# Kernel optimization log

Hardware: AMD Instinct MI355X
Metric: run time of the kernel (lower is better)

## Reference

```python
import jax, jax.numpy as jnp
import numpy as np
from jax import lax

BS, K, N = 8, 8, 16            # batch, gathers per sample, picks per curve
T, WG = 3072, 64               # gather time samples, traces
H, WC = 256, 256               # CVEncoder ScaleSize
RH, RW = 1024, 512             # resize (also GatherEncoder outLen=RH)
T0, T1 = 0.0, 7000.0           # tInt[0], tInt[-1]


def setup_inputs() -> dict:
    key = jax.random.key(0)
    ks = jax.random.split(key, 8)
    gather = jax.random.normal(ks[0], (BS, K, T, WG), jnp.float32)
    # cv: times sorted, strictly > 0, within [T0, T1]; velocities within VMM range
    times = jnp.sort(jax.random.uniform(ks[1], (BS, K, N), minval=100.0, maxval=T1), axis=-1)
    vels = jnp.sort(jax.random.uniform(ks[2], (BS, K, N), minval=1500.0, maxval=4500.0), axis=-1)
    cv = jnp.stack([times, vels], axis=-1).astype(jnp.float32)
    VMM = jnp.tile(jnp.array([1500.0, 4500.0], jnp.float32), (BS, 1))
    def cw(k, shape):
        return (jax.random.normal(k, shape, jnp.float32) * 0.1)
    params = dict(
        w1=cw(ks[3], (1, 1, 3, 3)), b1=jnp.zeros((1,), jnp.float32), g1=jnp.ones((1,), jnp.float32), be1=jnp.zeros((1,), jnp.float32),
        w2=cw(ks[4], (2, 3, 3, 3)), b2=jnp.zeros((2,), jnp.float32), g2=jnp.ones((2,), jnp.float32), be2=jnp.zeros((2,), jnp.float32),
        w3=cw(ks[5], (1, 2, 3, 2)), b3=jnp.zeros((1,), jnp.float32), g3=jnp.ones((1,), jnp.float32), be3=jnp.zeros((1,), jnp.float32),
        wf=cw(ks[6], (1, 1, 3, 3)), bf=jnp.zeros((1,), jnp.float32), gf=jnp.ones((1,), jnp.float32), bef=jnp.zeros((1,), jnp.float32),
    )
    return {"gather": gather, "cv": cv, "VMM": VMM, **params}


def _conv(x, w, b, stride, pad):
    y = lax.conv_general_dilated(x, w, stride, pad, dimension_numbers=("NCHW", "OIHW", "NCHW"))
    return y + b[None, :, None, None]


def _bn(x, g, b, eps=1e-5):
    # training-mode BatchNorm2d: stats over (N, H, W)
    m = jnp.mean(x, (0, 2, 3), keepdims=True)
    v = jnp.var(x, (0, 2, 3), keepdims=True)
    return (x - m) / jnp.sqrt(v + eps) * g[None, :, None, None] + b[None, :, None, None]


def _lrelu(x):
    return jnp.where(x >= 0, x, 0.1 * x)


def _cbl(x, w, b, g, be, stride):
    return _lrelu(_bn(_conv(x, w, b, stride, "VALID"), g, be))


def _maxpool(x, k):
    p = k // 2
    return lax.reduce_window(x, -jnp.inf, lax.max, (1, 1, k, k), (1, 1, 1, 1),
                             ((0, 0), (0, 0), (p, p), (p, p)))


def _cv_mask(cv, VMM):
    # normalize times to fractional row index and velocities to fractional col index
    dt = (T1 - T0) / (H - 1)
    t_idx = (cv[..., 0] - T0) / dt                                        # (BS,K,N)
    dv = (VMM[:, 1] - VMM[:, 0]) / (WC - 1)                               # (BS,)
    v_idx = (cv[..., 1] - VMM[:, 0, None, None]) / dv[:, None, None]      # (BS,K,N)
    t_flat = t_idx.reshape(-1, N)
    v_flat = v_idx.reshape(-1, N)
    tq = jnp.arange(H, dtype=jnp.float32)
    # per-curve piecewise-linear interpolation of v over the time grid
    v_curve = jax.vmap(lambda xp, fp: jnp.interp(tq, xp, fp))(t_flat, v_flat)  # (M,H)
    v_int = jnp.clip(v_curve.astype(jnp.int32), 0, WC - 1)
    M = BS * K
    mask = jnp.full((M, H, WC), 0.01, jnp.float32)
    mask = mask.at[jnp.arange(M)[:, None], jnp.arange(H)[None, :], v_int].add(0.9)
    mask = mask.reshape(BS, K, H, WC)
    # bilinear resize, half-pixel centers == torch align_corners=False
    return jax.image.resize(mask, (BS, K, RH, RW), method="linear")


def _forward(gather, cv, VMM, w1, b1, g1, be1, w2, b2, g2, be2, w3, b3, g3, be3, wf, bf, gf, bef):
    cv_mask = lax.stop_gradient(_cv_mask(cv, VMM))          # CVEncoder runs under no_grad
    x = gather.reshape(-1, 1, T, WG)                        # (BS*K,1,T,WG)
    x = x / jnp.max(jnp.abs(x))                             # mode='mute': keep sign
    x = _cbl(x, w1, b1, g1, be1, (3, 2))                    # (M,1,1024,31)
    xcat = jnp.concatenate([x, _maxpool(x, 3), _maxpool(x, 5)], axis=1)
    x = _cbl(xcat, w2, b2, g2, be2, (3, 2))                 # (M,2,341,15)
    x = _cbl(x, w3, b3, g3, be3, (3, 2))                    # (M,1,113,7)
    x = jax.image.resize(x, (x.shape[0], 1, RH, 1), method="linear")
    genr = x.reshape(BS, K, RH, 1)
    mix = jnp.sum(genr * cv_mask, axis=1, keepdims=True)    # (BS,1,RH,RW)
    y = _conv(mix, wf, bf, (1, 1), ((1, 1), (1, 1)))
    return _lrelu(_bn(y, gf, bef))


def reference(gather, cv, VMM, w1, b1, g1, be1, w2, b2, g2, be2, w3, b3, g3, be3, wf, bf, gf, bef):
    return _forward(gather, cv, VMM, w1, b1, g1, be1, w2, b2, g2, be2, w3, b3, g3, be3, wf, bf, gf, bef)
```

## Files before the change

kernel.cpp:

```cpp
#include <hip/hip_runtime.h>
#include <math.h>

#define BSZ 8
#define KG  8
#define NP  16
#define MM  64
#define TT  3072
#define WGN 64
#define HH  256
#define WCN 256
#define RHN 1024
#define RWN 512

#define C1H 1024
#define C1W 31
#define C2H 341
#define C2W 15
#define C3H 113
#define C3W 7

#define N1 (MM*C1H*C1W)
#define N2 (MM*C2H*C2W)
#define N3 (MM*C3H*C3W)
#define NF (BSZ*RHN*RWN)

#define SL 8

#define OFF_VINT 768
#define OFF_Y1   (OFF_VINT + MM*HH*4)
#define OFF_Y2   (OFF_Y1  + N1*4)
#define OFF_Y3   (OFF_Y2  + 2*N2*4)
#define OFF_GENR (OFF_Y3  + N3*4)

__device__ __forceinline__ void blockAdd2(double s, double ss, double* o0, double* o1) {
    __shared__ double red[4][2];
    __syncthreads();
    int lane = threadIdx.x & 63, wid = threadIdx.x >> 6;
#pragma unroll
    for (int off = 32; off > 0; off >>= 1) {
        s  += __shfl_down(s,  off, 64);
        ss += __shfl_down(ss, off, 64);
    }
    if (lane == 0) { red[wid][0] = s; red[wid][1] = ss; }
    __syncthreads();
    if (threadIdx.x == 0) {
        double a = 0, b = 0;
#pragma unroll
        for (int i = 0; i < 4; i++) { a += red[i][0]; b += red[i][1]; }
        int slot = blockIdx.x & (SL - 1);
        atomicAdd(&o0[slot], a); atomicAdd(&o1[slot], b);
    }
}

__device__ __forceinline__ float2 bn_ab(const double* __restrict__ sums, int c,
                                        const float* __restrict__ g,
                                        const float* __restrict__ be, double n) {
    double sum = 0, sumsq = 0;
#pragma unroll
    for (int j = 0; j < SL; j++) {
        sum   += sums[(2 * c) * SL + j];
        sumsq += sums[(2 * c + 1) * SL + j];
    }
    double mean = sum / n;
    double var  = sumsq / n - mean * mean;
    double a = (double)g[c] / sqrt(var + 1e-5);
    return make_float2((float)a, (float)((double)be[c] - mean * a));
}

__global__ void k_conv1(const float* __restrict__ g, const float* __restrict__ w1,
                        const float* __restrict__ b1,
                        float* __restrict__ y1, double* sums) {
    __shared__ float S[96][WGN];
    int tile = blockIdx.x;
    int m = tile >> 5, t32 = tile & 31;
    int oh0 = t32 * 32;
    const float4* g4 = (const float4*)(g + (size_t)m * TT * WGN + (size_t)(3 * oh0) * WGN);
    float4* s4 = (float4*)S;
#pragma unroll
    for (int i = threadIdx.x; i < 96 * WGN / 4; i += 256) s4[i] = g4[i];
    __syncthreads();
    float w[9];
#pragma unroll
    for (int i = 0; i < 9; i++) w[i] = w1[i];
    float bb = b1[0];
    double s = 0, ss = 0;
#pragma unroll
    for (int j = 0; j < 4; j++) {
        int o = threadIdx.x + j * 256;
        if (o < 32 * C1W) {
            int lo = o / C1W, ow = o % C1W;
            float acc = bb;
#pragma unroll
            for (int r = 0; r < 3; r++)
#pragma unroll
                for (int c = 0; c < 3; c++)
                    acc += w[r * 3 + c] * S[3 * lo + r][2 * ow + c];
            y1[(size_t)m * C1H * C1W + (size_t)(oh0 + lo) * C1W + ow] = acc;
            s += acc; ss += (double)acc * acc;
        }
    }
    blockAdd2(s, ss, &sums[0], &sums[SL]);
}

#define F2_OH 32
#define F2_NCH 11
#define F2_NRMAX (3*F2_OH + 4)
#define F2_PW 33
__global__ void k_fused2(const float* __restrict__ y1, const double* __restrict__ sums_r,
                         const float* __restrict__ g1, const float* __restrict__ be1,
                         const float* __restrict__ w2, const float* __restrict__ b2,
                         float* __restrict__ y2, double* sums) {
    __shared__ float sact[F2_NRMAX][F2_PW];
    __shared__ float sr3[F2_NRMAX][F2_PW];
    __shared__ float sr5[F2_NRMAX][F2_PW];
    float2 ab1 = bn_ab(sums_r, 0, g1, be1, (double)N1);
    int m   = blockIdx.x / F2_NCH;
    int ch  = blockIdx.x % F2_NCH;
    int oh0 = ch * F2_OH;
    int OHa = min(F2_OH, C2H - oh0);
    int NR  = 3 * OHa + 4;
    int gl0 = 3 * oh0 - 2;
    const float* yp = y1 + (size_t)m * C1H * C1W;
    for (int i = threadIdx.x; i < NR * C1W; i += blockDim.x) {
        int l = i / C1W, w = i % C1W;
        int gr = gl0 + l;
        float v = -INFINITY;
        if (gr >= 0 && gr < C1H) {
            v = ab1.x * yp[gr * C1W + w] + ab1.y;
            v = v >= 0.f ? v : 0.1f * v;
        }
        sact[l][w] = v;
    }
    __syncthreads();
    for (int i = threadIdx.x; i < NR * C1W; i += blockDim.x) {
        int l = i / C1W, w = i % C1W;
        int wl1 = max(w - 1, 0), wr1 = min(w + 1, C1W - 1);
        int wl2 = max(w - 2, 0), wr2 = min(w + 2, C1W - 1);
        float c  = sact[l][w];
        float m3 = fmaxf(fmaxf(sact[l][wl1], c), sact[l][wr1]);
        float m5 = fmaxf(fmaxf(m3, sact[l][wl2]), sact[l][wr2]);
        sr3[l][w] = m3;
        sr5[l][w] = m5;
    }
    __syncthreads();
    double s0 = 0, ss0 = 0, s1 = 0, ss1 = 0;
    for (int o = threadIdx.x; o < OHa * C2W; o += blockDim.x) {
        int lo = o / C2W, ow = o % C2W;
        float a0 = b2[0], acc1 = b2[1];
#pragma unroll
        for (int i = 0; i < 3; i++) {
            int l = 3 * lo + 2 + i;
#pragma unroll
            for (int j = 0; j < 3; j++) {
                int wc = 2 * ow + j;
                float v0 = sact[l][wc];
                float v1 = fmaxf(fmaxf(sr3[l - 1][wc], sr3[l][wc]), sr3[l + 1][wc]);
                float v2 = fmaxf(fmaxf(fmaxf(sr5[l - 2][wc], sr5[l - 1][wc]), sr5[l][wc]),
                                 fmaxf(sr5[l + 1][wc], sr5[l + 2][wc]));
                int ki = i * 3 + j;
                a0   += w2[ki] * v0 + w2[9 + ki] * v1 + w2[18 + ki] * v2;
                acc1 += w2[27 + ki] * v0 + w2[36 + ki] * v1 + w2[45 + ki] * v2;
            }
        }
        size_t ob = (size_t)m * (2 * C2H * C2W) + (size_t)(oh0 + lo) * C2W + ow;
        y2[ob] = a0;
        y2[ob + C2H * C2W] = acc1;
        s0 += a0; ss0 += (double)a0 * a0;
        s1 += acc1; ss1 += (double)acc1 * acc1;
    }
    blockAdd2(s0, ss0, &sums[2 * SL], &sums[3 * SL]);
    blockAdd2(s1, ss1, &sums[4 * SL], &sums[5 * SL]);
}

__global__ void k_conv3(const float* __restrict__ y2, const double* __restrict__ sums_r,
                        const float* __restrict__ g2, const float* __restrict__ be2,
                        const float* __restrict__ w3, const float* __restrict__ b3,
                        float* __restrict__ y3, double* sums) {
    float2 ab20 = bn_ab(sums_r + 2 * SL, 0, g2, be2, (double)N2);
    float2 ab21 = bn_ab(sums_r + 2 * SL, 1, g2, be2, (double)N2);
    double s = 0, ss = 0;
    int idx = blockIdx.x * blockDim.x + threadIdx.x;
    if (idx < N3) {
        int ow = idx % C3W;
        int t2 = idx / C3W;
        int oh = t2 % C3H;
        int m  = t2 / C3H;
        float acc = b3[0];
#pragma unroll
        for (int i = 0; i < 2; i++) {
            float aa = i ? ab21.x : ab20.x, bb = i ? ab21.y : ab20.y;
            const float* cp = y2 + (size_t)m * (2 * C2H * C2W) + (size_t)i * C2H * C2W
                              + (size_t)(oh * 3) * C2W + ow * 2;
#pragma unroll
            for (int r = 0; r < 3; r++)
#pragma unroll
                for (int c = 0; c < 2; c++) {
                    float v = aa * cp[r * C2W + c] + bb;
                    v = v >= 0.f ? v : 0.1f * v;
                    acc += w3[i * 6 + r * 2 + c] * v;
                }
        }
        y3[idx] = acc;
        s += acc; ss += (double)acc * acc;
    }
    blockAdd2(s, ss, &sums[6 * SL], &sums[7 * SL]);
}

__global__ void k_vintgenr(const float* __restrict__ cv, const float* __restrict__ VMM,
                           const float* __restrict__ y3, const double* __restrict__ sums_r,
                           const float* __restrict__ g3, const float* __restrict__ be3,
                           int* __restrict__ vint, float* __restrict__ genr) {
    __shared__ float tt[NP], vv[NP];
    __shared__ float tile[C3H * C3W];
    int m = blockIdx.x;
    int b = m >> 3;
    float2 ab3 = bn_ab(sums_r + 6 * SL, 0, g3, be3, (double)N3);
    if (threadIdx.x < NP) {
        int n = threadIdx.x;
        float t = cv[(m * NP + n) * 2 + 0];
        float v = cv[(m * NP + n) * 2 + 1];
        float dt = 7000.0f / 255.0f;
        tt[n] = t / dt;
        float vmin = VMM[b * 2], vmax = VMM[b * 2 + 1];
        float dv = (vmax - vmin) / 255.0f;
        vv[n] = (v - vmin) / dv;
    }
    for (int i = threadIdx.x; i < C3H * C3W; i += blockDim.x) {
        float v = ab3.x * y3[m * C3H * C3W + i] + ab3.y;
        tile[i] = v >= 0.f ? v : 0.1f * v;
    }
    __syncthreads();
    {
        int h = threadIdx.x;
        float x = (float)h;
        float val;
        if (x <= tt[0]) val = vv[0];
        else if (x >= tt[NP - 1]) val = vv[NP - 1];
        else {
            int i = 1;
            while (i < NP - 1 && tt[i] <= x) i++;
            float d = tt[i] - tt[i - 1];
            val = (d != 0.f) ? vv[i - 1] + (x - tt[i - 1]) / d * (vv[i] - vv[i - 1]) : vv[i];
        }
        int vi = (int)val;
        vint[m * HH + h] = max(0, min(WCN - 1, vi));
    }
    const float cwv[7] = { 4.f/37.f, 5.f/37.f, 6.f/37.f, 7.f/37.f,
                           6.f/37.f, 5.f/37.f, 4.f/37.f };
    for (int i = threadIdx.x; i < RHN; i += blockDim.x) {
        float sh = (i + 0.5f) * (113.0f / 1024.0f) - 0.5f;
        float fl = floorf(sh);
        float fr = sh - fl;
        int i0 = (int)fl, i1 = i0 + 1;
        i0 = max(0, min(C3H - 1, i0));
        i1 = max(0, min(C3H - 1, i1));
        float acc = 0.f;
#pragma unroll
        for (int x = 0; x < 7; x++) {
            float v = (1.f - fr) * tile[i0 * C3W + x] + fr * tile[i1 * C3W + x];
            acc += cwv[x] * v;
        }
        genr[m * RHN + i] = acc;
    }
}

#define MC_TH 16
__global__ void k_mixA(const float* __restrict__ genr, const int* __restrict__ vint,
                       const float* __restrict__ wf, const float* __restrict__ bf,
                       float* __restrict__ out, double* sums) {
    __shared__ float tile[MC_TH + 2][RWN + 2];
    __shared__ float Grow[MC_TH + 2];
    int b  = blockIdx.x / (RHN / MC_TH);
    int h0 = (blockIdx.x % (RHN / MC_TH)) * MC_TH;
    for (int i = threadIdx.x; i < (MC_TH + 2) * (RWN + 2); i += blockDim.x)
        ((float*)tile)[i] = 0.f;
    if (threadIdx.x < MC_TH + 2) Grow[threadIdx.x] = 0.f;
    __syncthreads();
    if (threadIdx.x < (MC_TH + 2) * KG) {
        int r = threadIdx.x / KG, k = threadIdx.x % KG;
        int h = h0 - 1 + r;
        if (h >= 0 && h < RHN) {
            int m = b * KG + k;
            float g = genr[m * RHN + h];
            atomicAdd(&Grow[r], g);
            float sh = (h + 0.5f) * 0.25f - 0.5f;
            float fl = floorf(sh);
            float fh = sh - fl;
            int ih0 = (int)fl, ih1 = ih0 + 1;
            ih0 = max(0, min(HH - 1, ih0));
            ih1 = max(0, min(HH - 1, ih1));
            int vv2[2] = { vint[m * HH + ih0], vint[m * HH + ih1] };
            float aa2[2] = { 0.9f * g * (1.f - fh), 0.9f * g * fh };
#pragma unroll
            for (int t = 0; t < 2; t++) {
                int v = vv2[t]; float A = aa2[t];
                if (v == 0) {
                    atomicAdd(&tile[r][1 + 0], A);
                    atomicAdd(&tile[r][1 + 1], 0.75f * A);
                    atomicAdd(&tile[r][1 + 2], 0.25f * A);
                } else if (v == WCN - 1) {
                    atomicAdd(&tile[r][1 + 509], 0.25f * A);
                    atomicAdd(&tile[r][1 + 510], 0.75f * A);
                    atomicAdd(&tile[r][1 + 511], A);
                } else {
                    atomicAdd(&tile[r][1 + 2 * v - 1], 0.25f * A);
                    atomicAdd(&tile[r][1 + 2 * v],     0.75f * A);
                    atomicAdd(&tile[r][1 + 2 * v + 1], 0.75f * A);
                    atomicAdd(&tile[r][1 + 2 * v + 2], 0.25f * A);
                }
            }
        }
    }
    __syncthreads();
    for (int i = threadIdx.x; i < (MC_TH + 2) * RWN; i += blockDim.x) {
        int r = i / RWN, w = i % RWN;
        int h = h0 - 1 + r;
        if (h >= 0 && h < RHN) tile[r][w + 1] += 0.01f * Grow[r];
    }
    __syncthreads();
    float w[9];
#pragma unroll
    for (int i = 0; i < 9; i++) w[i] = wf[i];
    float bb = bf[0];
    double s = 0, ss = 0;
#pragma unroll
    for (int j = 0; j < 32; j++) {
        int o  = threadIdx.x + j * 256;
        int lr = o >> 9, x = o & 511;
        float acc = bb;
#pragma unroll
        for (int dr = 0; dr < 3; dr++)
#pragma unroll
            for (int dc = 0; dc < 3; dc++)
                acc += w[dr * 3 + dc] * tile[lr + dr][x + dc];
        out[((size_t)b * RHN + (h0 + lr)) * RWN + x] = acc;
        s += acc; ss += (double)acc * acc;
    }
    blockAdd2(s, ss, &sums[8 * SL], &sums[9 * SL]);
}

__global__ void k_act4(float4* __restrict__ x, const double* __restrict__ sums_r,
                       const float* __restrict__ gf, const float* __restrict__ bef) {
    float2 abf = bn_ab(sums_r + 8 * SL, 0, gf, bef, (double)NF);
    int i = blockIdx.x * blockDim.x + threadIdx.x;
    float a = abf.x, b = abf.y;
    float4 v = x[i];
    v.x = a * v.x + b; v.x = v.x >= 0.f ? v.x : 0.1f * v.x;
    v.y = a * v.y + b; v.y = v.y >= 0.f ? v.y : 0.1f * v.y;
    v.z = a * v.z + b; v.z = v.z >= 0.f ? v.z : 0.1f * v.z;
    v.w = a * v.w + b; v.w = v.w >= 0.f ? v.w : 0.1f * v.w;
    x[i] = v;
}

extern "C" void kernel_launch(void* const* d_in, const int* in_sizes, int n_in,
                              void* d_out, int out_size, void* d_ws, size_t ws_size,
                              hipStream_t stream) {
    const float* gather = (const float*)d_in[0];
    const float* cv     = (const float*)d_in[1];
    const float* VMM    = (const float*)d_in[2];
    const float* w1 = (const float*)d_in[3];
    const float* b1 = (const float*)d_in[4];
    const float* g1 = (const float*)d_in[5];
    const float* be1 = (const float*)d_in[6];
    const float* w2 = (const float*)d_in[7];
    const float* b2 = (const float*)d_in[8];
    const float* g2 = (const float*)d_in[9];
    const float* be2 = (const float*)d_in[10];
    const float* w3 = (const float*)d_in[11];
    const float* b3 = (const float*)d_in[12];
    const float* g3 = (const float*)d_in[13];
    const float* be3 = (const float*)d_in[14];
    const float* wf = (const float*)d_in[15];
    const float* bf = (const float*)d_in[16];
    const float* gf = (const float*)d_in[17];
    const float* bef = (const float*)d_in[18];
    float* out = (float*)d_out;

    char* ws = (char*)d_ws;
    double* sums = (double*)ws;
    int*   vint  = (int*)(ws + OFF_VINT);
    float* y1    = (float*)(ws + OFF_Y1);
    float* y2    = (float*)(ws + OFF_Y2);
    float* y3    = (float*)(ws + OFF_Y3);
    float* genr  = (float*)(ws + OFF_GENR);

    hipMemsetAsync(d_ws, 0, 640, stream);

    k_conv1<<<MM * 32, 256, 0, stream>>>(gather, w1, b1, y1, sums);
    k_fused2<<<MM * F2_NCH, 256, 0, stream>>>(y1, sums, g1, be1, w2, b2, y2, sums);
    k_conv3<<<(N3 + 255) / 256, 256, 0, stream>>>(y2, sums, g2, be2, w3, b3, y3, sums);
    k_vintgenr<<<MM, 256, 0, stream>>>(cv, VMM, y3, sums, g3, be3, vint, genr);
    k_mixA<<<BSZ * (RHN / MC_TH), 256, 0, stream>>>(genr, vint, wf, bf, out, sums);
    k_act4<<<NF / 4 / 256, 256, 0, stream>>>((float4*)out, sums, gf, bef);
}
```

Before: 202.8 us.

## Recompute mix tile in two passes instead of storing and re-reading output

Removes the separate vint/genr kernel by computing the resized encoder value and the curve velocity index inline inside the mix kernels. The final conv output is no longer written and then re-read by a separate activation pass. Instead a stats-only pass (k_mixA) accumulates BN sums, and a second pass (k_mixB) rebuilds the same tile, redoes the conv, and applies BN plus LeakyReLU before a single write. This trades a 16 MB store-and-reload round trip and one launch for duplicated tile construction and convolution work.

After: 210.7 us. 1.04x slower.

```diff
diff --git a/kernel.cpp b/kernel.cpp
--- a/kernel.cpp
+++ b/kernel.cpp
@@ -26,11 +26,9 @@
 
 #define SL 8
 
-#define OFF_VINT 768
-#define OFF_Y1   (OFF_VINT + MM*HH*4)
-#define OFF_Y2   (OFF_Y1  + N1*4)
-#define OFF_Y3   (OFF_Y2  + 2*N2*4)
-#define OFF_GENR (OFF_Y3  + N3*4)
+#define OFF_Y1   768
+#define OFF_Y2   (OFF_Y1 + N1*4)
+#define OFF_Y3   (OFF_Y2 + 2*N2*4)
 
 __device__ __forceinline__ void blockAdd2(double s, double ss, double* o0, double* o1) {
     __shared__ double red[4][2];
@@ -206,82 +204,55 @@
     blockAdd2(s, ss, &sums[6 * SL], &sums[7 * SL]);
 }
 
-__global__ void k_vintgenr(const float* __restrict__ cv, const float* __restrict__ VMM,
-                           const float* __restrict__ y3, const double* __restrict__ sums_r,
-                           const float* __restrict__ g3, const float* __restrict__ be3,
-                           int* __restrict__ vint, float* __restrict__ genr) {
-    __shared__ float tt[NP], vv[NP];
-    __shared__ float tile[C3H * C3W];
-    int m = blockIdx.x;
-    int b = m >> 3;
-    float2 ab3 = bn_ab(sums_r + 6 * SL, 0, g3, be3, (double)N3);
-    if (threadIdx.x < NP) {
-        int n = threadIdx.x;
-        float t = cv[(m * NP + n) * 2 + 0];
-        float v = cv[(m * NP + n) * 2 + 1];
-        float dt = 7000.0f / 255.0f;
-        tt[n] = t / dt;
-        float vmin = VMM[b * 2], vmax = VMM[b * 2 + 1];
-        float dv = (vmax - vmin) / 255.0f;
-        vv[n] = (v - vmin) / dv;
-    }
-    for (int i = threadIdx.x; i < C3H * C3W; i += blockDim.x) {
-        float v = ab3.x * y3[m * C3H * C3W + i] + ab3.y;
-        tile[i] = v >= 0.f ? v : 0.1f * v;
-    }
-    __syncthreads();
-    {
-        int h = threadIdx.x;
-        float x = (float)h;
-        float val;
-        if (x <= tt[0]) val = vv[0];
-        else if (x >= tt[NP - 1]) val = vv[NP - 1];
-        else {
-            int i = 1;
-            while (i < NP - 1 && tt[i] <= x) i++;
-            float d = tt[i] - tt[i - 1];
-            val = (d != 0.f) ? vv[i - 1] + (x - tt[i - 1]) / d * (vv[i] - vv[i - 1]) : vv[i];
-        }
-        int vi = (int)val;
-        vint[m * HH + h] = max(0, min(WCN - 1, vi));
-    }
-    const float cwv[7] = { 4.f/37.f, 5.f/37.f, 6.f/37.f, 7.f/37.f,
-                           6.f/37.f, 5.f/37.f, 4.f/37.f };
-    for (int i = threadIdx.x; i < RHN; i += blockDim.x) {
-        float sh = (i + 0.5f) * (113.0f / 1024.0f) - 0.5f;
-        float fl = floorf(sh);
-        float fr = sh - fl;
-        int i0 = (int)fl, i1 = i0 + 1;
-        i0 = max(0, min(C3H - 1, i0));
-        i1 = max(0, min(C3H - 1, i1));
-        float acc = 0.f;
-#pragma unroll
-        for (int x = 0; x < 7; x++) {
-            float v = (1.f - fr) * tile[i0 * C3W + x] + fr * tile[i1 * C3W + x];
-            acc += cwv[x] * v;
-        }
-        genr[m * RHN + i] = acc;
-    }
+__device__ __forceinline__ float curve_at(const float* tt, const float* vv, float x) {
+    if (x <= tt[0]) return vv[0];
+    if (x >= tt[NP - 1]) return vv[NP - 1];
+    int i = 1;
+    while (i < NP - 1 && tt[i] <= x) i++;
+    float d = tt[i] - tt[i - 1];
+    return (d != 0.f) ? vv[i - 1] + (x - tt[i - 1]) / d * (vv[i] - vv[i - 1]) : vv[i];
 }
 
 #define MC_TH 16
-__global__ void k_mixA(const float* __restrict__ genr, const int* __restrict__ vint,
-                       const float* __restrict__ wf, const float* __restrict__ bf,
-                       float* __restrict__ out, double* sums) {
-    __shared__ float tile[MC_TH + 2][RWN + 2];
-    __shared__ float Grow[MC_TH + 2];
-    int b  = blockIdx.x / (RHN / MC_TH);
-    int h0 = (blockIdx.x % (RHN / MC_TH)) * MC_TH;
+__device__ __forceinline__ void build_mix_tile(
+        const float* __restrict__ cv, const float* __restrict__ VMM,
+        const float* __restrict__ y3, float2 ab3,
+        int b, int h0, float (*tile)[RWN + 2], float* Grow,
+        float (*sTT)[NP], float (*sVV)[NP]) {
     for (int i = threadIdx.x; i < (MC_TH + 2) * (RWN + 2); i += blockDim.x)
         ((float*)tile)[i] = 0.f;
     if (threadIdx.x < MC_TH + 2) Grow[threadIdx.x] = 0.f;
+    if (threadIdx.x < KG * NP) {
+        int k = threadIdx.x / NP, n = threadIdx.x % NP;
+        int m = b * KG + k;
+        float t = cv[(m * NP + n) * 2 + 0];
+        float v = cv[(m * NP + n) * 2 + 1];
+        sTT[k][n] = t * (255.0f / 7000.0f);
+        float vmin = VMM[b * 2], vmax = VMM[b * 2 + 1];
+        sVV[k][n] = (v - vmin) * (255.0f / (vmax - vmin));
+    }
     __syncthreads();
     if (threadIdx.x < (MC_TH + 2) * KG) {
         int r = threadIdx.x / KG, k = threadIdx.x % KG;
         int h = h0 - 1 + r;
         if (h >= 0 && h < RHN) {
             int m = b * KG + k;
-            float g = genr[m * RHN + h];
+            const float cwv[7] = { 4.f/37.f, 5.f/37.f, 6.f/37.f, 7.f/37.f,
+                                   6.f/37.f, 5.f/37.f, 4.f/37.f };
+            float shg = (h + 0.5f) * (113.0f / 1024.0f) - 0.5f;
+            float flg = floorf(shg);
+            float fr  = shg - flg;
+            int i0 = (int)flg, i1 = i0 + 1;
+            i0 = max(0, min(C3H - 1, i0));
+            i1 = max(0, min(C3H - 1, i1));
+            const float* yp = y3 + (size_t)m * C3H * C3W;
+            float g = 0.f;
+#pragma unroll
+            for (int x = 0; x < 7; x++) {
+                float va = ab3.x * yp[i0 * C3W + x] + ab3.y; va = va >= 0.f ? va : 0.1f * va;
+                float vb = ab3.x * yp[i1 * C3W + x] + ab3.y; vb = vb >= 0.f ? vb : 0.1f * vb;
+                g += cwv[x] * ((1.f - fr) * va + fr * vb);
+            }
             atomicAdd(&Grow[r], g);
             float sh = (h + 0.5f) * 0.25f - 0.5f;
             float fl = floorf(sh);
@@ -289,7 +260,9 @@
             int ih0 = (int)fl, ih1 = ih0 + 1;
             ih0 = max(0, min(HH - 1, ih0));
             ih1 = max(0, min(HH - 1, ih1));
-            int vv2[2] = { vint[m * HH + ih0], vint[m * HH + ih1] };
+            int vv2[2];
+            vv2[0] = max(0, min(WCN - 1, (int)curve_at(sTT[k], sVV[k], (float)ih0)));
+            vv2[1] = max(0, min(WCN - 1, (int)curve_at(sTT[k], sVV[k], (float)ih1)));
             float aa2[2] = { 0.9f * g * (1.f - fh), 0.9f * g * fh };
 #pragma unroll
             for (int t = 0; t < 2; t++) {
@@ -318,6 +291,20 @@
         if (h >= 0 && h < RHN) tile[r][w + 1] += 0.01f * Grow[r];
     }
     __syncthreads();
+}
+
+__global__ void k_mixA(const float* __restrict__ cv, const float* __restrict__ VMM,
+                       const float* __restrict__ y3, const double* __restrict__ sums_r,
+                       const float* __restrict__ g3, const float* __restrict__ be3,
+                       const float* __restrict__ wf, const float* __restrict__ bf,
+                       double* sums) {
+    __shared__ float tile[MC_TH + 2][RWN + 2];
+    __shared__ float Grow[MC_TH + 2];
+    __shared__ float sTT[KG][NP], sVV[KG][NP];
+    float2 ab3 = bn_ab(sums_r + 6 * SL, 0, g3, be3, (double)N3);
+    int b  = blockIdx.x / (RHN / MC_TH);
+    int h0 = (blockIdx.x % (RHN / MC_TH)) * MC_TH;
+    build_mix_tile(cv, VMM, y3, ab3, b, h0, tile, Grow, sTT, sVV);
     float w[9];
 #pragma unroll
     for (int i = 0; i < 9; i++) w[i] = wf[i];
@@ -333,23 +320,42 @@
 #pragma unroll
             for (int dc = 0; dc < 3; dc++)
                 acc += w[dr * 3 + dc] * tile[lr + dr][x + dc];
-        out[((size_t)b * RHN + (h0 + lr)) * RWN + x] = acc;
         s += acc; ss += (double)acc * acc;
     }
     blockAdd2(s, ss, &sums[8 * SL], &sums[9 * SL]);
 }
 
-__global__ void k_act4(float4* __restrict__ x, const double* __restrict__ sums_r,
-                       const float* __restrict__ gf, const float* __restrict__ bef) {
+__global__ void k_mixB(const float* __restrict__ cv, const float* __restrict__ VMM,
+                       const float* __restrict__ y3, const double* __restrict__ sums_r,
+                       const float* __restrict__ g3, const float* __restrict__ be3,
+                       const float* __restrict__ wf, const float* __restrict__ bf,
+                       const float* __restrict__ gf, const float* __restrict__ bef,
+                       float* __restrict__ out) {
+    __shared__ float tile[MC_TH + 2][RWN + 2];
+    __shared__ float Grow[MC_TH + 2];
+    __shared__ float sTT[KG][NP], sVV[KG][NP];
+    float2 ab3 = bn_ab(sums_r + 6 * SL, 0, g3, be3, (double)N3);
     float2 abf = bn_ab(sums_r + 8 * SL, 0, gf, bef, (double)NF);
-    int i = blockIdx.x * blockDim.x + threadIdx.x;
-    float a = abf.x, b = abf.y;
-    float4 v = x[i];
-    v.x = a * v.x + b; v.x = v.x >= 0.f ? v.x : 0.1f * v.x;
-    v.y = a * v.y + b; v.y = v.y >= 0.f ? v.y : 0.1f * v.y;
-    v.z = a * v.z + b; v.z = v.z >= 0.f ? v.z : 0.1f * v.z;
-    v.w = a * v.w + b; v.w = v.w >= 0.f ? v.w : 0.1f * v.w;
-    x[i] = v;
+    int b  = blockIdx.x / (RHN / MC_TH);
+    int h0 = (blockIdx.x % (RHN / MC_TH)) * MC_TH;
+    build_mix_tile(cv, VMM, y3, ab3, b, h0, tile, Grow, sTT, sVV);
+    float w[9];
+#pragma unroll
+    for (int i = 0; i < 9; i++) w[i] = wf[i];
+    float bb = bf[0];
+#pragma unroll
+    for (int j = 0; j < 32; j++) {
+        int o  = threadIdx.x + j * 256;
+        int lr = o >> 9, x = o & 511;
+        float acc = bb;
+#pragma unroll
+        for (int dr = 0; dr < 3; dr++)
+#pragma unroll
+            for (int dc = 0; dc < 3; dc++)
+                acc += w[dr * 3 + dc] * tile[lr + dr][x + dc];
+        float v = abf.x * acc + abf.y;
+        out[((size_t)b * RHN + (h0 + lr)) * RWN + x] = v >= 0.f ? v : 0.1f * v;
+    }
 }
 
 extern "C" void kernel_launch(void* const* d_in, const int* in_sizes, int n_in,
@@ -378,18 +384,16 @@
 
     char* ws = (char*)d_ws;
     double* sums = (double*)ws;
-    int*   vint  = (int*)(ws + OFF_VINT);
     float* y1    = (float*)(ws + OFF_Y1);
     float* y2    = (float*)(ws + OFF_Y2);
     float* y3    = (float*)(ws + OFF_Y3);
-    float* genr  = (float*)(ws + OFF_GENR);
 
     hipMemsetAsync(d_ws, 0, 640, stream);
 
     k_conv1<<<MM * 32, 256, 0, stream>>>(gather, w1, b1, y1, sums);
     k_fused2<<<MM * F2_NCH, 256, 0, stream>>>(y1, sums, g1, be1, w2, b2, y2, sums);
     k_conv3<<<(N3 + 255) / 256, 256, 0, stream>>>(y2, sums, g2, be2, w3, b3, y3, sums);
-    k_vintgenr<<<MM, 256, 0, stream>>>(cv, VMM, y3, sums, g3, be3, vint, genr);
-    k_mixA<<<BSZ * (RHN / MC_TH), 256, 0, stream>>>(genr, vint, wf, bf, out, sums);
-    k_act4<<<NF / 4 / 256, 256, 0, stream>>>((float4*)out, sums, gf, bef);
-}
+    k_mixA<<<BSZ * (RHN / MC_TH), 256, 0, stream>>>(cv, VMM, y3, sums, g3, be3, wf, bf, sums);
+    k_mixB<<<BSZ * (RHN / MC_TH), 256, 0, stream>>>(cv, VMM, y3, sums, g3, be3, wf, bf,
+                                                    gf, bef, out);
+}
```
